# Performance work log

Hardware: AMD Instinct MI355X
Metric: run time of the kernel (lower is better)

Reference implementation:

```python
import jax, jax.numpy as jnp
import numpy as np

N, E, C, D, M = 20000, 640000, 128, 128, 128


def setup_inputs() -> dict:
    key = jax.random.key(0)
    ks = jax.random.split(key, 16)
    g = lambda k, shape, fan: jax.random.normal(k, shape, jnp.float32) * (1.0 / np.sqrt(fan))
    return {
        "x": jax.random.normal(ks[0], (N, C), jnp.float32),
        "edge_index": jax.random.randint(ks[1], (2, E), 0, N, jnp.int64),
        "W_src": g(ks[2], (C, D), C),
        "b_src": jnp.zeros((D,), jnp.float32),
        "W_tgt": g(ks[3], (C, D), C),
        "W_skip": g(ks[4], (C, D), C),
        "a0": jnp.asarray(0.2, jnp.float32),   # PReLU init=0.2
        "W1": g(ks[5], (D, M), D),
        "b1": jnp.zeros((M,), jnp.float32),
        "a1": jnp.asarray(0.25, jnp.float32),  # MLP PReLU default
        "W2": g(ks[6], (M, D), M),
        "b2": jnp.zeros((D,), jnp.float32),
        "Wg": g(ks[7], (D, 1), D),
        "gamma": jnp.ones((D,), jnp.float32),
        "beta": jnp.zeros((D,), jnp.float32),
    }


def _prelu(h, a):
    return jnp.where(h >= 0, h, a * h)


def reference(x, edge_index, W_src, b_src, W_tgt, W_skip, a0, W1, b1, a1, W2, b2, Wg, gamma, beta):
    n = x.shape[0]
    j, i = edge_index[0], edge_index[1]  # src -> tgt
    msg_src = x @ W_src + b_src          # lin_src (bias)
    msg_tgt = x @ W_tgt                  # lin_tgt (no bias)
    # per-edge message: msg_nn(msg_j + msg_i) = PReLU -> Linear -> PReLU -> Linear
    h = _prelu(msg_src[j] + msg_tgt[i], a0)          # [E, D]
    h = _prelu(h @ W1 + b1, a1)                      # [E, M]
    msg = h @ W2 + b2                                # [E, D]
    # gate + sparse softmax over edges grouped by target node i
    gate = msg @ Wg                                  # [E, 1]
    gmax = jax.ops.segment_max(gate, i, num_segments=n)
    eg = jnp.exp(gate - gmax[i])
    gsum = jax.ops.segment_sum(eg, i, num_segments=n)
    alpha = eg / (gsum[i] + 1e-16)                   # [E, 1]
    # aggregate (aggr='add')
    out = jax.ops.segment_sum(alpha * msg, i, num_segments=n)  # [N, D]
    # root/skip connection
    out = out + x @ W_skip
    # LayerNorm
    mu = jnp.mean(out, axis=-1, keepdims=True)
    var = jnp.var(out, axis=-1, keepdims=True)
    out = (out - mu) * jax.lax.rsqrt(var + 1e-5) * gamma + beta
    return out
```

## Files before the change

kernel.cpp:

```cpp
#include <hip/hip_runtime.h>
#include <hip/hip_bf16.h>
#include <stdint.h>

#define DIM 128
#define HSTR 136
#define H2STR 72
#define NPB 16
#define NMAX 20224

using hfrag = __attribute__((ext_vector_type(8))) _Float16;
using h2v   = __attribute__((ext_vector_type(2))) _Float16;
using f32x4 = __attribute__((ext_vector_type(4))) float;

__device__ __forceinline__ float prelu_f(float v, float a) { return v >= 0.f ? v : a * v; }

__device__ __forceinline__ unsigned pkh(float a, float b) {
    auto h = __builtin_amdgcn_cvt_pkrtz(a, b);
    return *(unsigned*)&h;
}
__device__ __forceinline__ unsigned short hs(float v) {
    _Float16 h = (_Float16)v;
    return *(unsigned short*)&h;
}
__device__ __forceinline__ unsigned prelu2_add(unsigned su, unsigned gu, h2v a2) {
    h2v s = *(h2v*)&su, g = *(h2v*)&gu;
    h2v h = s + g;
    h2v z = {(_Float16)0.f, (_Float16)0.f};
    h2v mx = __builtin_elementwise_max(h, z);
    h2v mn = __builtin_elementwise_min(h, z);
    h2v r = mn * a2 + mx;
    return *(unsigned*)&r;
}

__global__ __launch_bounds__(256) void prep_hist_k(
    const float* __restrict__ Wsrc, const float* __restrict__ Wtgt,
    const float* __restrict__ Wskip, const float* __restrict__ W1,
    const float* __restrict__ W2, const float* __restrict__ b2,
    const float* __restrict__ Wg,
    unsigned short* __restrict__ Wall, float* __restrict__ w2g,
    const int* __restrict__ eidx, int E, int* __restrict__ deg,
    int* __restrict__ rank)
{
    const int nhist = (E + 255) / 256;
    if ((int)blockIdx.x < nhist) {
        const int e = blockIdx.x * 256 + threadIdx.x;
        if (e < E) rank[e] = atomicAdd(deg + eidx[(size_t)E + e], 1);
        return;
    }
    const int b = blockIdx.x - nhist;
    if (b == (5 * DIM * DIM) / 256) {
        const int k = threadIdx.x;
        if (k < DIM) {
            float s = 0.f;
            for (int d = 0; d < DIM; ++d) s += W2[k * DIM + d] * Wg[d];
            w2g[k] = s;
        } else if (k == DIM) {
            float s = 0.f;
            for (int d = 0; d < DIM; ++d) s += b2[d] * Wg[d];
            w2g[DIM] = s;
        }
        return;
    }
    const int idx = b * 256 + threadIdx.x;
    const int m = idx >> 14;
    const int r = idx & 16383;
    const int n = r >> 7, k = r & 127;
    const float* W = (m == 0) ? Wsrc : (m == 1) ? Wtgt : (m == 2) ? Wskip : (m == 3) ? W1 : W2;
    const _Float16 hv = (_Float16)W[k * DIM + n];
    Wall[idx] = *(const unsigned short*)&hv;
}

__global__ __launch_bounds__(1024) void scan_k(const int* __restrict__ deg,
                                               int* __restrict__ rowptr, int N)
{
    __shared__ int part[1024];
    const int t = threadIdx.x;

    if (N <= NMAX) {
        __shared__ int s[NMAX];
        for (int k = t; k < N; k += 1024) s[k] = deg[k];
        __syncthreads();

        const int chunk = (N + 1023) / 1024;
        const int lo = min(t * chunk, N), hi = min(lo + chunk, N);
        int sum = 0;
        for (int k = lo; k < hi; ++k) sum += s[k];
        part[t] = sum;
        __syncthreads();
        for (int off = 1; off < 1024; off <<= 1) {
            int u = (t >= off) ? part[t - off] : 0;
            __syncthreads();
            part[t] += u;
            __syncthreads();
        }
        int run = part[t] - sum;
        for (int k = lo; k < hi; ++k) { const int d = s[k]; s[k] = run; run += d; }
        __syncthreads();
        for (int k = t; k < N; k += 1024) rowptr[k] = s[k];
        if (t == 0) rowptr[N] = part[1023];
    } else {
        const int chunk = (N + 1023) / 1024;
        const int lo = min(t * chunk, N), hi = min(lo + chunk, N);
        int s = 0;
        for (int k = lo; k < hi; ++k) s += deg[k];
        part[t] = s;
        __syncthreads();
        for (int off = 1; off < 1024; off <<= 1) {
            int u = (t >= off) ? part[t - off] : 0;
            __syncthreads();
            part[t] += u;
            __syncthreads();
        }
        int run = part[t] - s;
        for (int k = lo; k < hi; ++k) {
            rowptr[k] = run;
            run += deg[k];
        }
        if (t == 1023) rowptr[N] = part[1023];
    }
}

__global__ __launch_bounds__(256) void scatter_node_k(
    const int* __restrict__ eidx, int E,
    const int* __restrict__ rowptr, const int* __restrict__ rank,
    int2* __restrict__ jip, int nscatter,
    const float* __restrict__ x,
    const unsigned short* __restrict__ Wall,
    const float* __restrict__ bsrc,
    unsigned short* __restrict__ msg_src, unsigned short* __restrict__ msg_tgt,
    float* __restrict__ skip, int N)
{
    if ((int)blockIdx.x < nscatter) {
        const int e = blockIdx.x * 256 + threadIdx.x;
        if (e < E) {
            const int j = eidx[e];
            const int i = eidx[(size_t)E + e];
            const int p = rowptr[i] + rank[e];
            jip[p] = make_int2(j, i);
        }
        return;
    }

    __shared__ unsigned short xt[32 * HSTR];
    const int t = threadIdx.x;
    const int n0blk = (blockIdx.x - nscatter) * 32;
    const int w = t >> 6, lane = t & 63, col = lane & 15, quad = lane >> 4;

    for (int k = t; k < 32 * 16; k += 256) {
        const int row = k >> 4, o = k & 15;
        uint4 v = make_uint4(0, 0, 0, 0);
        if (n0blk + row < N) {
            const float4 a = *(const float4*)(x + (size_t)(n0blk + row) * DIM + o * 8);
            const float4 b = *(const float4*)(x + (size_t)(n0blk + row) * DIM + o * 8 + 4);
            v.x = pkh(a.x, a.y); v.y = pkh(a.z, a.w);
            v.z = pkh(b.x, b.y); v.w = pkh(b.z, b.w);
        }
        *(uint4*)(xt + row * HSTR + o * 8) = v;
    }
    __syncthreads();

    hfrag af[2][4];
    #pragma unroll
    for (int mt = 0; mt < 2; ++mt)
        #pragma unroll
        for (int ks = 0; ks < 4; ++ks)
            af[mt][ks] = *(const hfrag*)(xt + (mt * 16 + col) * HSTR + ks * 32 + quad * 8);

    for (int m = 0; m < 3; ++m) {
        const unsigned short* Wt = Wall + m * DIM * DIM;
        hfrag bw[2][4];
        #pragma unroll
        for (int nt = 0; nt < 2; ++nt)
            #pragma unroll
            for (int ks = 0; ks < 4; ++ks)
                bw[nt][ks] = *(const hfrag*)(Wt + (w * 32 + nt * 16 + col) * DIM + ks * 32 + quad * 8);

        f32x4 acc[2][2];
        #pragma unroll
        for (int mt = 0; mt < 2; ++mt)
            #pragma unroll
            for (int nt = 0; nt < 2; ++nt)
                acc[mt][nt] = f32x4{0.f, 0.f, 0.f, 0.f};

        #pragma unroll
        for (int mt = 0; mt < 2; ++mt)
            #pragma unroll
            for (int nt = 0; nt < 2; ++nt)
                #pragma unroll
                for (int ks = 0; ks < 4; ++ks)
                    acc[mt][nt] = __builtin_amdgcn_mfma_f32_16x16x32_f16(
                        bw[nt][ks], af[mt][ks], acc[mt][nt], 0, 0, 0);

        #pragma unroll
        for (int mt = 0; mt < 2; ++mt) {
            const int node = n0blk + mt * 16 + col;
            if (node >= N) continue;
            #pragma unroll
            for (int nt = 0; nt < 2; ++nt) {
                const int f0 = w * 32 + nt * 16 + quad * 4;
                if (m == 2) {
                    float4 o;
                    o.x = acc[mt][nt][0]; o.y = acc[mt][nt][1];
                    o.z = acc[mt][nt][2]; o.w = acc[mt][nt][3];
                    *(float4*)(skip + (size_t)node * DIM + f0) = o;
                } else {
                    float b0 = 0.f, b1v = 0.f, b2v = 0.f, b3v = 0.f;
                    if (m == 0) {
                        const float4 bb = *(const float4*)(bsrc + f0);
                        b0 = bb.x; b1v = bb.y; b2v = bb.z; b3v = bb.w;
                    }
                    uint2 o;
                    o.x = pkh(acc[mt][nt][0] + b0, acc[mt][nt][1] + b1v);
                    o.y = pkh(acc[mt][nt][2] + b2v, acc[mt][nt][3] + b3v);
                    unsigned short* dst = (m == 0) ? msg_src : msg_tgt;
                    *(uint2*)(dst + (size_t)node * DIM + f0) = o;
                }
            }
        }
    }
}

__global__ __launch_bounds__(256, 2) void edge_fused_node(
    const int2* __restrict__ jip, const int* __restrict__ rowptr, int N,
    const unsigned short* __restrict__ msg_src, const unsigned short* __restrict__ msg_tgt,
    const float* __restrict__ a0p,
    const unsigned short* __restrict__ W1t, const float* __restrict__ b1,
    const float* __restrict__ a1p,
    const float* __restrict__ w2g,
    unsigned short* __restrict__ aggh2)
{
    __shared__ unsigned short h1[64 * HSTR];
    __shared__ unsigned short h2t[DIM * H2STR];
    __shared__ unsigned short tgt_lds[NPB * HSTR];
    __shared__ float gate_part[4][64];
    __shared__ int il_lds[2][64];

    const int t = threadIdx.x;
    const float a0 = *a0p, a1 = *a1p;
    const h2v a02 = {(_Float16)a0, (_Float16)a0};
    const int w = t >> 6, lane = t & 63, col = lane & 15, quad = lane >> 4;
    const int o = t & 15, r0 = t >> 4;

    const int n0 = blockIdx.x * NPB;
    const int elo = rowptr[n0];
    const int ehi = rowptr[min(n0 + NPB, N)];
    const int tc = (ehi - elo + 63) >> 6;

    hfrag bw1[2][4];
    float4 b1q[2], wgq[2];
    #pragma unroll
    for (int nt = 0; nt < 2; ++nt) {
        const int n = w * 32 + nt * 16 + col;
        #pragma unroll
        for (int ks = 0; ks < 4; ++ks)
            bw1[nt][ks] = *(const hfrag*)(W1t + n * DIM + ks * 32 + quad * 8);
        const int nq = w * 32 + nt * 16 + quad * 4;
        b1q[nt] = *(const float4*)(b1 + nq);
        wgq[nt] = *(const float4*)(w2g + nq);
    }
    const float c2 = w2g[DIM];

    for (int k = t; k < NPB * 16; k += 256) {
        const int row = k >> 4, oo = k & 15;
        const int node = n0 + row;
        uint4 v = make_uint4(0, 0, 0, 0);
        if (node < N) v = *(const uint4*)(msg_tgt + (size_t)node * DIM + oo * 8);
        *(uint4*)(tgt_lds + row * HSTR + oo * 8) = v;
    }
    __syncthreads();

    f32x4 acc2[2] = {f32x4{0.f, 0.f, 0.f, 0.f}, f32x4{0.f, 0.f, 0.f, 0.f}};
    float zreg = 0.f;

    if (tc > 0) {
        {
            int2 e0r[4];
            #pragma unroll
            for (int i = 0; i < 4; ++i)
                e0r[i] = jip[min(elo + r0 + 16 * i, ehi - 1)];
            #pragma unroll
            for (int i = 0; i < 4; ++i) {
                const uint4 sv = *(const uint4*)(msg_src + (size_t)e0r[i].x * DIM + o * 8);
                const uint4 gv = *(const uint4*)(tgt_lds + (e0r[i].y - n0) * HSTR + o * 8);
                uint4 hv;
                hv.x = prelu2_add(sv.x, gv.x, a02);
                hv.y = prelu2_add(sv.y, gv.y, a02);
                hv.z = prelu2_add(sv.z, gv.z, a02);
                hv.w = prelu2_add(sv.w, gv.w, a02);
                *(uint4*)(h1 + (r0 + 16 * i) * HSTR + o * 8) = hv;
                if (o == 0) il_lds[0][r0 + 16 * i] = e0r[i].y;
            }
        }
        int2 eN[4];
        {
            const int t1 = min(1, tc - 1);
            #pragma unroll
            for (int i = 0; i < 4; ++i)
                eN[i] = jip[min(elo + t1 * 64 + r0 + 16 * i, ehi - 1)];
        }

        int par = 0;

        for (int tt = 0; tt < tc; ++tt) {
            __syncthreads();

            const bool pf = (tt + 1 < tc);

            uint4 sv[4];
            if (pf) {
                #pragma unroll
                for (int i = 0; i < 4; ++i)
                    sv[i] = *(const uint4*)(msg_src + (size_t)eN[i].x * DIM + o * 8);
            }

            f32x4 acc[4][2];
            #pragma unroll
            for (int mt = 0; mt < 4; ++mt)
                #pragma unroll
                for (int nt = 0; nt < 2; ++nt)
                    acc[mt][nt] = f32x4{0.f, 0.f, 0.f, 0.f};

            __builtin_amdgcn_s_setprio(1);
            #pragma unroll
            for (int mt = 0; mt < 4; ++mt) {
                hfrag af[4];
                #pragma unroll
                for (int ks = 0; ks < 4; ++ks)
                    af[ks] = *(const hfrag*)(h1 + (mt * 16 + col) * HSTR + ks * 32 + quad * 8);
                #pragma unroll
                for (int nt = 0; nt < 2; ++nt)
                    #pragma unroll
                    for (int ks = 0; ks < 4; ++ks)
                        acc[mt][nt] = __builtin_amdgcn_mfma_f32_16x16x32_f16(
                            bw1[nt][ks], af[ks], acc[mt][nt], 0, 0, 0);
            }
            __builtin_amdgcn_s_setprio(0);

            #pragma unroll
            for (int mt = 0; mt < 4; ++mt) {
                const int m = mt * 16 + col;
                float g = 0.f;
                #pragma unroll
                for (int nt = 0; nt < 2; ++nt) {
                    const int fb = w * 32 + nt * 16 + quad * 4;
                    const float p0v = prelu_f(acc[mt][nt][0] + b1q[nt].x, a1);
                    const float p1v = prelu_f(acc[mt][nt][1] + b1q[nt].y, a1);
                    const float p2v = prelu_f(acc[mt][nt][2] + b1q[nt].z, a1);
                    const float p3v = prelu_f(acc[mt][nt][3] + b1q[nt].w, a1);
                    h2t[(fb + 0) * H2STR + m] = hs(p0v);
                    h2t[(fb + 1) * H2STR + m] = hs(p1v);
                    h2t[(fb + 2) * H2STR + m] = hs(p2v);
                    h2t[(fb + 3) * H2STR + m] = hs(p3v);
                    g += p0v * wgq[nt].x + p1v * wgq[nt].y + p2v * wgq[nt].z + p3v * wgq[nt].w;
                }
                g += __shfl_xor(g, 16);
                g += __shfl_xor(g, 32);
                if (quad == 0) gate_part[w][m] = g;
            }

            __syncthreads();

            if (pf) {
                #pragma unroll
                for (int i = 0; i < 4; ++i) {
                    const uint4 gv = *(const uint4*)(tgt_lds + (eN[i].y - n0) * HSTR + o * 8);
                    uint4 hv;
                    hv.x = prelu2_add(sv[i].x, gv.x, a02);
                    hv.y = prelu2_add(sv[i].y, gv.y, a02);
                    hv.z = prelu2_add(sv[i].z, gv.z, a02);
                    hv.w = prelu2_add(sv[i].w, gv.w, a02);
                    *(uint4*)(h1 + (r0 + 16 * i) * HSTR + o * 8) = hv;
                    if (o == 0) il_lds[par ^ 1][r0 + 16 * i] = eN[i].y;
                }
                const int t2 = min(tt + 2, tc - 1);
                #pragma unroll
                for (int i = 0; i < 4; ++i)
                    eN[i] = jip[min(elo + t2 * 64 + r0 + 16 * i, ehi - 1)];
            }

            {
                const int ebase = elo + tt * 64;
                const int limit = min(64, ehi - ebase);
                hfrag bf2[2];
                float zp = 0.f;
                #pragma unroll
                for (int ks = 0; ks < 2; ++ks) {
                    const int e0 = ks * 32 + quad * 8;
                    const float4 ga0 = *(const float4*)&gate_part[0][e0];
                    const float4 ga1 = *(const float4*)&gate_part[1][e0];
                    const float4 ga2 = *(const float4*)&gate_part[2][e0];
                    const float4 ga3 = *(const float4*)&gate_part[3][e0];
                    const float4 gb0 = *(const float4*)&gate_part[0][e0 + 4];
                    const float4 gb1 = *(const float4*)&gate_part[1][e0 + 4];
                    const float4 gb2 = *(const float4*)&gate_part[2][e0 + 4];
                    const float4 gb3 = *(const float4*)&gate_part[3][e0 + 4];
                    const int4 ia = *(const int4*)&il_lds[par][e0];
                    const int4 ib = *(const int4*)&il_lds[par][e0 + 4];
                    const float e0v = __expf(fminf(ga0.x + ga1.x + ga2.x + ga3.x + c2, 11.f));
                    const float e1v = __expf(fminf(ga0.y + ga1.y + ga2.y + ga3.y + c2, 11.f));
                    const float e2v = __expf(fminf(ga0.z + ga1.z + ga2.z + ga3.z + c2, 11.f));
                    const float e3v = __expf(fminf(ga0.w + ga1.w + ga2.w + ga3.w + c2, 11.f));
                    const float e4v = __expf(fminf(gb0.x + gb1.x + gb2.x + gb3.x + c2, 11.f));
                    const float e5v = __expf(fminf(gb0.y + gb1.y + gb2.y + gb3.y + c2, 11.f));
                    const float e6v = __expf(fminf(gb0.z + gb1.z + gb2.z + gb3.z + c2, 11.f));
                    const float e7v = __expf(fminf(gb0.w + gb1.w + gb2.w + gb3.w + c2, 11.f));
                    const float s0 = (ia.x - n0 == col && e0 + 0 < limit) ? e0v : 0.f;
                    const float s1 = (ia.y - n0 == col && e0 + 1 < limit) ? e1v : 0.f;
                    const float s2 = (ia.z - n0 == col && e0 + 2 < limit) ? e2v : 0.f;
                    const float s3 = (ia.w - n0 == col && e0 + 3 < limit) ? e3v : 0.f;
                    const float s4 = (ib.x - n0 == col && e0 + 4 < limit) ? e4v : 0.f;
                    const float s5 = (ib.y - n0 == col && e0 + 5 < limit) ? e5v : 0.f;
                    const float s6 = (ib.z - n0 == col && e0 + 6 < limit) ? e6v : 0.f;
                    const float s7 = (ib.w - n0 == col && e0 + 7 < limit) ? e7v : 0.f;
                    zp += s0 + s1 + s2 + s3 + s4 + s5 + s6 + s7;
                    uint4 uu;
                    uu.x = pkh(s0, s1); uu.y = pkh(s2, s3);
                    uu.z = pkh(s4, s5); uu.w = pkh(s6, s7);
                    bf2[ks] = *(hfrag*)&uu;
                }
                float z = zp;
                z += __shfl_xor(z, 16);
                z += __shfl_xor(z, 32);
                zreg += z;
                #pragma unroll
                for (int nt = 0; nt < 2; ++nt)
                    #pragma unroll
                    for (int ks = 0; ks < 2; ++ks) {
                        const hfrag a2 = *(const hfrag*)(
                            h2t + (w * 32 + nt * 16 + col) * H2STR + ks * 32 + quad * 8);
                        acc2[nt] = __builtin_amdgcn_mfma_f32_16x16x32_f16(
                            a2, bf2[ks], acc2[nt], 0, 0, 0);
                    }
            }

            par ^= 1;
        }
    }

    const int node = n0 + col;
    if (node < N) {
        const float invz = 1.f / (zreg + 1e-16f);
        #pragma unroll
        for (int nt = 0; nt < 2; ++nt) {
            uint2 ov;
            ov.x = pkh(acc2[nt][0] * invz, acc2[nt][1] * invz);
            ov.y = pkh(acc2[nt][2] * invz, acc2[nt][3] * invz);
            *(uint2*)(aggh2 + (size_t)node * DIM + w * 32 + nt * 16 + quad * 4) = ov;
        }
    }
}

__global__ __launch_bounds__(256) void node_out_k(
    const unsigned short* __restrict__ aggh2,
    const unsigned short* __restrict__ W2t, const float* __restrict__ b2,
    const float* __restrict__ skip,
    const float* __restrict__ gamma, const float* __restrict__ beta,
    float* __restrict__ out, int N)
{
    __shared__ unsigned short hh[64 * HSTR];
    __shared__ float ls1[4][4][16], ls2[4][4][16];

    const int t = threadIdx.x;
    const int n0blk = blockIdx.x * 64;
    const int w = t >> 6, lane = t & 63, col = lane & 15, quad = lane >> 4;

    hfrag bw2[2][4];
    float4 b2q[2];
    #pragma unroll
    for (int nt = 0; nt < 2; ++nt) {
        const int n = w * 32 + nt * 16 + col;
        #pragma unroll
        for (int ks = 0; ks < 4; ++ks)
            bw2[nt][ks] = *(const hfrag*)(W2t + n * DIM + ks * 32 + quad * 8);
        b2q[nt] = *(const float4*)(b2 + w * 32 + nt * 16 + quad * 4);
    }

    for (int k = t; k < 64 * 16; k += 256) {
        const int row = k >> 4, oo = k & 15;
        uint4 v = make_uint4(0, 0, 0, 0);
        if (n0blk + row < N) v = *(const uint4*)(aggh2 + (size_t)(n0blk + row) * DIM + oo * 8);
        *(uint4*)(hh + row * HSTR + oo * 8) = v;
    }
    __syncthreads();

    f32x4 acc[4][2];
    #pragma unroll
    for (int mt = 0; mt < 4; ++mt)
        #pragma unroll
        for (int nt = 0; nt < 2; ++nt)
            acc[mt][nt] = f32x4{0.f, 0.f, 0.f, 0.f};

    #pragma unroll
    for (int mt = 0; mt < 4; ++mt) {
        hfrag af[4];
        #pragma unroll
        for (int ks = 0; ks < 4; ++ks)
            af[ks] = *(const hfrag*)(hh + (mt * 16 + col) * HSTR + ks * 32 + quad * 8);
        #pragma unroll
        for (int nt = 0; nt < 2; ++nt)
            #pragma unroll
            for (int ks = 0; ks < 4; ++ks)
                acc[mt][nt] = __builtin_amdgcn_mfma_f32_16x16x32_f16(
                    bw2[nt][ks], af[ks], acc[mt][nt], 0, 0, 0);
    }

    float v[4][2][4];
    #pragma unroll
    for (int mt = 0; mt < 4; ++mt) {
        const int node = n0blk + mt * 16 + col;
        float s1 = 0.f, s2 = 0.f;
        #pragma unroll
        for (int nt = 0; nt < 2; ++nt) {
            const int f0 = w * 32 + nt * 16 + quad * 4;
            float4 sk = make_float4(0.f, 0.f, 0.f, 0.f);
            if (node < N) sk = *(const float4*)(skip + (size_t)node * DIM + f0);
            v[mt][nt][0] = acc[mt][nt][0] + b2q[nt].x + sk.x;
            v[mt][nt][1] = acc[mt][nt][1] + b2q[nt].y + sk.y;
            v[mt][nt][2] = acc[mt][nt][2] + b2q[nt].z + sk.z;
            v[mt][nt][3] = acc[mt][nt][3] + b2q[nt].w + sk.w;
            #pragma unroll
            for (int r = 0; r < 4; ++r) {
                s1 += v[mt][nt][r];
                s2 += v[mt][nt][r] * v[mt][nt][r];
            }
        }
        s1 += __shfl_xor(s1, 16); s1 += __shfl_xor(s1, 32);
        s2 += __shfl_xor(s2, 16); s2 += __shfl_xor(s2, 32);
        if (quad == 0) { ls1[w][mt][col] = s1; ls2[w][mt][col] = s2; }
    }
    __syncthreads();

    #pragma unroll
    for (int mt = 0; mt < 4; ++mt) {
        const int node = n0blk + mt * 16 + col;
        if (node >= N) continue;
        const float sum = ls1[0][mt][col] + ls1[1][mt][col] + ls1[2][mt][col] + ls1[3][mt][col];
        const float sq  = ls2[0][mt][col] + ls2[1][mt][col] + ls2[2][mt][col] + ls2[3][mt][col];
        const float mu = sum * (1.f / 128.f);
        const float var = sq * (1.f / 128.f) - mu * mu;
        const float rs = rsqrtf(var + 1e-5f);
        #pragma unroll
        for (int nt = 0; nt < 2; ++nt) {
            const int f0 = w * 32 + nt * 16 + quad * 4;
            const float4 gm = *(const float4*)(gamma + f0);
            const float4 bt = *(const float4*)(beta + f0);
            float4 ov;
            ov.x = (v[mt][nt][0] - mu) * rs * gm.x + bt.x;
            ov.y = (v[mt][nt][1] - mu) * rs * gm.y + bt.y;
            ov.z = (v[mt][nt][2] - mu) * rs * gm.z + bt.z;
            ov.w = (v[mt][nt][3] - mu) * rs * gm.w + bt.w;
            *(float4*)(out + (size_t)node * DIM + f0) = ov;
        }
    }
}

extern "C" void kernel_launch(void* const* d_in, const int* in_sizes, int n_in,
                              void* d_out, int out_size, void* d_ws, size_t ws_size,
                              hipStream_t stream)
{
    const float* x     = (const float*)d_in[0];
    const int*   eidx  = (const int*)d_in[1];
    const float* Wsrc  = (const float*)d_in[2];
    const float* bsrc  = (const float*)d_in[3];
    const float* Wtgt  = (const float*)d_in[4];
    const float* Wskip = (const float*)d_in[5];
    const float* a0    = (const float*)d_in[6];
    const float* W1    = (const float*)d_in[7];
    const float* b1    = (const float*)d_in[8];
    const float* a1    = (const float*)d_in[9];
    const float* W2    = (const float*)d_in[10];
    const float* b2    = (const float*)d_in[11];
    const float* Wg    = (const float*)d_in[12];
    const float* gamma = (const float*)d_in[13];
    const float* beta  = (const float*)d_in[14];

    const int N = in_sizes[0] / DIM;
    const int E = in_sizes[1] / 2;
    const int Npad = ((N + 63) / 64) * 64;
    float* out = (float*)d_out;

    char* ws = (char*)d_ws;
    size_t off = 0;
    auto alloc = [&](size_t bytes) -> void* {
        void* p = ws + off;
        off += (bytes + 255) & ~(size_t)255;
        return p;
    };
    int*            deg     = (int*)alloc((size_t)N * 4);
    unsigned short* msg_src = (unsigned short*)alloc((size_t)N * DIM * 2);
    unsigned short* msg_tgt = (unsigned short*)alloc((size_t)N * DIM * 2);
    float*          skip    = (float*)alloc((size_t)N * DIM * 4);
    int*            rowptr  = (int*)alloc((size_t)(N + 1) * 4);
    int*            rank    = (int*)alloc((size_t)E * 4);
    int2*           jip     = (int2*)alloc((size_t)E * 8);
    unsigned short* Wall    = (unsigned short*)alloc((size_t)5 * DIM * DIM * 2);
    float*          w2g     = (float*)alloc((size_t)(DIM + 1) * 4);
    unsigned short* aggh2   = (unsigned short*)alloc((size_t)Npad * DIM * 2);
    (void)ws_size; (void)n_in; (void)out_size;

    (void)hipMemsetAsync(deg, 0, (size_t)N * 4, stream);

    const int nhist = (E + 255) / 256;
    prep_hist_k<<<nhist + (5 * DIM * DIM) / 256 + 1, 256, 0, stream>>>(
        Wsrc, Wtgt, Wskip, W1, W2, b2, Wg, Wall, w2g, eidx, E, deg, rank);

    scan_k<<<1, 1024, 0, stream>>>(deg, rowptr, N);

    const int nscatter = (E + 255) / 256;
    const int nnode = (N + 31) / 32;
    scatter_node_k<<<nscatter + nnode, 256, 0, stream>>>(
        eidx, E, rowptr, rank, jip, nscatter,
        x, Wall, bsrc, msg_src, msg_tgt, skip, N);

    const int nblk = (N + NPB - 1) / NPB;
    edge_fused_node<<<nblk, 256, 0, stream>>>(jip, rowptr, N, msg_src, msg_tgt, a0,
                                              Wall + 3 * DIM * DIM, b1, a1,
                                              w2g, aggh2);

    node_out_k<<<Npad / 64, 256, 0, stream>>>(aggh2, Wall + 4 * DIM * DIM, b2, skip,
                                              gamma, beta, out, N);
}
```

Baseline: 250.1 us.

## Fuse node output GEMM and LayerNorm into edge kernel epilogue

The separate node_out_k kernel is removed. Its W2 projection, skip add and LayerNorm now run in the epilogue of edge_fused_node on the 16-node tile, with the aggregated fp16 h2 staged in shared memory instead of a global aggh2 buffer. This drops one kernel launch and the global write and read of the intermediate. In exchange the edge kernel carries extra register pressure from the W2 fragments, and each block issues only one 16-row MFMA tile, which may hurt occupancy in the main loop.

```diff
diff --git a/kernel.cpp b/kernel.cpp
--- a/kernel.cpp
+++ b/kernel.cpp
@@ -227,7 +227,10 @@
     const unsigned short* __restrict__ W1t, const float* __restrict__ b1,
     const float* __restrict__ a1p,
     const float* __restrict__ w2g,
-    unsigned short* __restrict__ aggh2)
+    const unsigned short* __restrict__ W2t, const float* __restrict__ b2,
+    const float* __restrict__ skip,
+    const float* __restrict__ gamma, const float* __restrict__ beta,
+    float* __restrict__ out)
 {
     __shared__ unsigned short h1[64 * HSTR];
     __shared__ unsigned short h2t[DIM * H2STR];
@@ -437,32 +440,18 @@
         }
     }
 
-    const int node = n0 + col;
-    if (node < N) {
+    unsigned short* agg_lds = h1;
+    {
         const float invz = 1.f / (zreg + 1e-16f);
         #pragma unroll
         for (int nt = 0; nt < 2; ++nt) {
             uint2 ov;
             ov.x = pkh(acc2[nt][0] * invz, acc2[nt][1] * invz);
             ov.y = pkh(acc2[nt][2] * invz, acc2[nt][3] * invz);
-            *(uint2*)(aggh2 + (size_t)node * DIM + w * 32 + nt * 16 + quad * 4) = ov;
-        }
-    }
-}
-
-__global__ __launch_bounds__(256) void node_out_k(
-    const unsigned short* __restrict__ aggh2,
-    const unsigned short* __restrict__ W2t, const float* __restrict__ b2,
-    const float* __restrict__ skip,
-    const float* __restrict__ gamma, const float* __restrict__ beta,
-    float* __restrict__ out, int N)
-{
-    __shared__ unsigned short hh[64 * HSTR];
-    __shared__ float ls1[4][4][16], ls2[4][4][16];
-
-    const int t = threadIdx.x;
-    const int n0blk = blockIdx.x * 64;
-    const int w = t >> 6, lane = t & 63, col = lane & 15, quad = lane >> 4;
+            *(uint2*)(agg_lds + col * HSTR + w * 32 + nt * 16 + quad * 4) = ov;
+        }
+    }
+    __syncthreads();
 
     hfrag bw2[2][4];
     float4 b2q[2];
@@ -475,67 +464,47 @@
         b2q[nt] = *(const float4*)(b2 + w * 32 + nt * 16 + quad * 4);
     }
 
-    for (int k = t; k < 64 * 16; k += 256) {
-        const int row = k >> 4, oo = k & 15;
-        uint4 v = make_uint4(0, 0, 0, 0);
-        if (n0blk + row < N) v = *(const uint4*)(aggh2 + (size_t)(n0blk + row) * DIM + oo * 8);
-        *(uint4*)(hh + row * HSTR + oo * 8) = v;
-    }
+    hfrag afo[4];
+    #pragma unroll
+    for (int ks = 0; ks < 4; ++ks)
+        afo[ks] = *(const hfrag*)(agg_lds + col * HSTR + ks * 32 + quad * 8);
+
+    f32x4 accO[2] = {f32x4{0.f, 0.f, 0.f, 0.f}, f32x4{0.f, 0.f, 0.f, 0.f}};
+    #pragma unroll
+    for (int nt = 0; nt < 2; ++nt)
+        #pragma unroll
+        for (int ks = 0; ks < 4; ++ks)
+            accO[nt] = __builtin_amdgcn_mfma_f32_16x16x32_f16(
+                bw2[nt][ks], afo[ks], accO[nt], 0, 0, 0);
+
+    const int node = n0 + col;
+    float v[2][4];
+    float s1 = 0.f, s2 = 0.f;
+    #pragma unroll
+    for (int nt = 0; nt < 2; ++nt) {
+        const int f0 = w * 32 + nt * 16 + quad * 4;
+        float4 sk = make_float4(0.f, 0.f, 0.f, 0.f);
+        if (node < N) sk = *(const float4*)(skip + (size_t)node * DIM + f0);
+        v[nt][0] = accO[nt][0] + b2q[nt].x + sk.x;
+        v[nt][1] = accO[nt][1] + b2q[nt].y + sk.y;
+        v[nt][2] = accO[nt][2] + b2q[nt].z + sk.z;
+        v[nt][3] = accO[nt][3] + b2q[nt].w + sk.w;
+        #pragma unroll
+        for (int r = 0; r < 4; ++r) {
+            s1 += v[nt][r];
+            s2 += v[nt][r] * v[nt][r];
+        }
+    }
+    s1 += __shfl_xor(s1, 16); s1 += __shfl_xor(s1, 32);
+    s2 += __shfl_xor(s2, 16); s2 += __shfl_xor(s2, 32);
+    if (quad == 0) { gate_part[w][col] = s1; gate_part[w][16 + col] = s2; }
     __syncthreads();
 
-    f32x4 acc[4][2];
-    #pragma unroll
-    for (int mt = 0; mt < 4; ++mt)
-        #pragma unroll
-        for (int nt = 0; nt < 2; ++nt)
-            acc[mt][nt] = f32x4{0.f, 0.f, 0.f, 0.f};
-
-    #pragma unroll
-    for (int mt = 0; mt < 4; ++mt) {
-        hfrag af[4];
-        #pragma unroll
-        for (int ks = 0; ks < 4; ++ks)
-            af[ks] = *(const hfrag*)(hh + (mt * 16 + col) * HSTR + ks * 32 + quad * 8);
-        #pragma unroll
-        for (int nt = 0; nt < 2; ++nt)
-            #pragma unroll
-            for (int ks = 0; ks < 4; ++ks)
-                acc[mt][nt] = __builtin_amdgcn_mfma_f32_16x16x32_f16(
-                    bw2[nt][ks], af[ks], acc[mt][nt], 0, 0, 0);
-    }
-
-    float v[4][2][4];
-    #pragma unroll
-    for (int mt = 0; mt < 4; ++mt) {
-        const int node = n0blk + mt * 16 + col;
-        float s1 = 0.f, s2 = 0.f;
-        #pragma unroll
-        for (int nt = 0; nt < 2; ++nt) {
-            const int f0 = w * 32 + nt * 16 + quad * 4;
-            float4 sk = make_float4(0.f, 0.f, 0.f, 0.f);
-            if (node < N) sk = *(const float4*)(skip + (size_t)node * DIM + f0);
-            v[mt][nt][0] = acc[mt][nt][0] + b2q[nt].x + sk.x;
-            v[mt][nt][1] = acc[mt][nt][1] + b2q[nt].y + sk.y;
-            v[mt][nt][2] = acc[mt][nt][2] + b2q[nt].z + sk.z;
-            v[mt][nt][3] = acc[mt][nt][3] + b2q[nt].w + sk.w;
-            #pragma unroll
-            for (int r = 0; r < 4; ++r) {
-                s1 += v[mt][nt][r];
-                s2 += v[mt][nt][r] * v[mt][nt][r];
-            }
-        }
-        s1 += __shfl_xor(s1, 16); s1 += __shfl_xor(s1, 32);
-        s2 += __shfl_xor(s2, 16); s2 += __shfl_xor(s2, 32);
-        if (quad == 0) { ls1[w][mt][col] = s1; ls2[w][mt][col] = s2; }
-    }
-    __syncthreads();
-
-    #pragma unroll
-    for (int mt = 0; mt < 4; ++mt) {
-        const int node = n0blk + mt * 16 + col;
-        if (node >= N) continue;
-        const float sum = ls1[0][mt][col] + ls1[1][mt][col] + ls1[2][mt][col] + ls1[3][mt][col];
-        const float sq  = ls2[0][mt][col] + ls2[1][mt][col] + ls2[2][mt][col] + ls2[3][mt][col];
+    if (node < N) {
+        const float sum = gate_part[0][col] + gate_part[1][col]
+                        + gate_part[2][col] + gate_part[3][col];
+        const float sq  = gate_part[0][16 + col] + gate_part[1][16 + col]
+                        + gate_part[2][16 + col] + gate_part[3][16 + col];
         const float mu = sum * (1.f / 128.f);
         const float var = sq * (1.f / 128.f) - mu * mu;
         const float rs = rsqrtf(var + 1e-5f);
@@ -545,10 +514,10 @@
             const float4 gm = *(const float4*)(gamma + f0);
             const float4 bt = *(const float4*)(beta + f0);
             float4 ov;
-            ov.x = (v[mt][nt][0] - mu) * rs * gm.x + bt.x;
-            ov.y = (v[mt][nt][1] - mu) * rs * gm.y + bt.y;
-            ov.z = (v[mt][nt][2] - mu) * rs * gm.z + bt.z;
-            ov.w = (v[mt][nt][3] - mu) * rs * gm.w + bt.w;
+            ov.x = (v[nt][0] - mu) * rs * gm.x + bt.x;
+            ov.y = (v[nt][1] - mu) * rs * gm.y + bt.y;
+            ov.z = (v[nt][2] - mu) * rs * gm.z + bt.z;
+            ov.w = (v[nt][3] - mu) * rs * gm.w + bt.w;
             *(float4*)(out + (size_t)node * DIM + f0) = ov;
         }
     }
@@ -576,7 +545,6 @@
 
     const int N = in_sizes[0] / DIM;
     const int E = in_sizes[1] / 2;
-    const int Npad = ((N + 63) / 64) * 64;
     float* out = (float*)d_out;
 
     char* ws = (char*)d_ws;
@@ -595,7 +563,6 @@
     int2*           jip     = (int2*)alloc((size_t)E * 8);
     unsigned short* Wall    = (unsigned short*)alloc((size_t)5 * DIM * DIM * 2);
     float*          w2g     = (float*)alloc((size_t)(DIM + 1) * 4);
-    unsigned short* aggh2   = (unsigned short*)alloc((size_t)Npad * DIM * 2);
     (void)ws_size; (void)n_in; (void)out_size;
 
     (void)hipMemsetAsync(deg, 0, (size_t)N * 4, stream);
@@ -614,9 +581,7 @@
 
     const int nblk = (N + NPB - 1) / NPB;
     edge_fused_node<<<nblk, 256, 0, stream>>>(jip, rowptr, N, msg_src, msg_tgt, a0,
-                                              Wall + 3 * DIM * DIM, b1, a1,
-                                              w2g, aggh2);
-
-    node_out_k<<<Npad / 64, 256, 0, stream>>>(aggh2, Wall + 4 * DIM * DIM, b2, skip,
-                                              gamma, beta, out, N);
-}
+                                              Wall + 3 * DIM * DIM, b1, a1, w2g,
+                                              Wall + 4 * DIM * DIM, b2, skip,
+                                              gamma, beta, out);
+}
```

New measurement: 245.9 us. No clear change (-1.7%).
